# Kernel tuning notes

Hardware: AMD Instinct MI355X
Metric: run time of the kernel (lower is better)

The kernel has to match this reference:

```python
import jax, jax.numpy as jnp
import numpy as np

NUM_TAGS = 16
PAD, START, STOP = 0, 14, 15
EMBED, HIDDEN = 300, 300
HALF = HIDDEN // 2  # per-direction hidden size
B, T, VOCAB = 64, 512, 50000
NEG = -10000.0


def _lstm_dir(x, mask, Wih, Whh, bih, bhh, reverse):
    # x: (B,T,D) float, mask: (B,T) float 0/1. Mask-gated state emulates packed sequences.
    h0 = jnp.zeros((x.shape[0], Whh.shape[1]), x.dtype)

    def step(carry, inp):
        h, c = carry
        xt, mt = inp
        gates = xt @ Wih.T + bih + h @ Whh.T + bhh  # (B, 4*HALF)
        i, f, g, o = jnp.split(gates, 4, axis=-1)  # torch gate order i,f,g,o
        c_new = jax.nn.sigmoid(f) * c + jax.nn.sigmoid(i) * jnp.tanh(g)
        h_new = jax.nn.sigmoid(o) * jnp.tanh(c_new)
        m = mt[:, None]
        h = m * h_new + (1.0 - m) * h
        c = m * c_new + (1.0 - m) * c
        return (h, c), h

    xs = (jnp.swapaxes(x, 0, 1), jnp.swapaxes(mask, 0, 1))
    _, hs = jax.lax.scan(step, (h0, h0), xs, reverse=reverse)
    return jnp.swapaxes(hs, 0, 1)  # (B,T,HALF)


def _bilstm(x, mask, Wih, Whh, bih, bhh):
    fwd = _lstm_dir(x, mask, Wih[0], Whh[0], bih[0], bhh[0], False)
    bwd = _lstm_dir(x, mask, Wih[1], Whh[1], bih[1], bhh[1], True)
    return jnp.concatenate([fwd, bwd], axis=-1)  # (B,T,HIDDEN)


def _crf_partition(h, mask, trans):
    # Forward algorithm: log-sum-exp recurrence over tags.
    alpha = jnp.full((h.shape[0], NUM_TAGS), NEG, h.dtype).at[:, START].set(0.0)

    def step(alpha, inp):
        ht, mt = inp  # ht: (B,K), mt: (B,)
        # scores[b, next, prev] = alpha[b,prev] + emission[b,next] + trans[next,prev]
        a_new = jax.nn.logsumexp(alpha[:, None, :] + ht[:, :, None] + trans[None], axis=-1)
        m = mt[:, None]
        return a_new * m + alpha * (1.0 - m), None

    alpha, _ = jax.lax.scan(step, alpha, (jnp.swapaxes(h, 0, 1), jnp.swapaxes(mask, 0, 1)))
    return jax.nn.logsumexp(alpha + trans[STOP], axis=-1)  # (B,)


def _crf_score(h, y, mask, trans):
    # Gold path score, fully vectorized (original loops per batch element).
    b = h.shape[0]
    y_ext = jnp.concatenate([jnp.full((b, 1), START, dtype=y.dtype), y], axis=1)  # (B,T+1)
    em = jnp.take_along_axis(h, y_ext[:, 1:, None], axis=2)[..., 0]  # (B,T)
    tr = trans[y_ext[:, 1:], y_ext[:, :-1]]  # (B,T)
    score = jnp.sum((em + tr) * mask, axis=1)
    lengths = jnp.sum(mask, axis=1).astype(jnp.int32)
    last = jnp.take_along_axis(y_ext, lengths[:, None], axis=1)[:, 0]
    return score + trans[STOP, last]


def _forward(x, y, embed_weight, Wih0, Whh0, bih0, bhh0, Wih1, Whh1, bih1, bhh1, Wout, bout, transition):
    mask = (x > 0).astype(jnp.float32)
    e = embed_weight[x]  # (B,T,EMBED); PAD row is zeros
    h1 = _bilstm(e, mask, Wih0, Whh0, bih0, bhh0)
    h2 = _bilstm(h1, mask, Wih1, Whh1, bih1, bhh1)
    emis = (h2 @ Wout.T + bout) * mask[..., None]  # (B,T,NUM_TAGS)
    Z = _crf_partition(emis, mask, transition)
    s = _crf_score(emis, y, mask, transition)
    return Z - s  # per-example NLL, shape (B,)


def setup_inputs():
    key = jax.random.key(0)
    ks = jax.random.split(key, 16)
    lengths = jax.random.randint(ks[0], (B,), T // 4, T + 1)
    mask = jnp.arange(T)[None, :] < lengths[:, None]
    x = jnp.where(mask, jax.random.randint(ks[1], (B, T), 1, VOCAB), 0).astype(jnp.int32)
    y = jnp.where(mask, jax.random.randint(ks[2], (B, T), 1, 14), 0).astype(jnp.int32)
    embed_weight = jax.random.normal(ks[3], (VOCAB, EMBED), jnp.float32).at[PAD].set(0.0)
    s = 1.0 / float(np.sqrt(HALF))

    def u(k, shape):
        return jax.random.uniform(k, shape, jnp.float32, -s, s)

    Wih0 = u(ks[4], (2, 4 * HALF, EMBED))
    Whh0 = u(ks[5], (2, 4 * HALF, HALF))
    bih0 = u(ks[6], (2, 4 * HALF))
    bhh0 = u(ks[7], (2, 4 * HALF))
    Wih1 = u(ks[8], (2, 4 * HALF, HIDDEN))
    Whh1 = u(ks[9], (2, 4 * HALF, HALF))
    bih1 = u(ks[10], (2, 4 * HALF))
    bhh1 = u(ks[11], (2, 4 * HALF))
    Wout = u(ks[12], (NUM_TAGS, HIDDEN))
    bout = u(ks[13], (NUM_TAGS,))
    tr = jax.random.normal(ks[14], (NUM_TAGS, NUM_TAGS), jnp.float32)
    tr = tr.at[START, :].set(NEG).at[:, STOP].set(NEG).at[:, PAD].set(NEG).at[PAD, :].set(NEG)
    tr = tr.at[PAD, STOP].set(0.0).at[PAD, PAD].set(0.0)
    return {"x": x, "y": y, "embed_weight": embed_weight,
            "Wih0": Wih0, "Whh0": Whh0, "bih0": bih0, "bhh0": bhh0,
            "Wih1": Wih1, "Whh1": Whh1, "bih1": bih1, "bhh1": bhh1,
            "Wout": Wout, "bout": bout, "transition": tr}


def reference(x, y, embed_weight, Wih0, Whh0, bih0, bhh0, Wih1, Whh1, bih1, bhh1, Wout, bout, transition):
    return _forward(x, y, embed_weight, Wih0, Whh0, bih0, bhh0, Wih1, Whh1, bih1, bhh1, Wout, bout, transition)
```

## Files before the change

### kernel.cpp

```cpp
#include <hip/hip_runtime.h>
#include <hip/hip_bf16.h>

#define TB 512
#define NB 64
#define HID 300
#define HHALF 150
#define G4 600
#define KP 320
#define MTOT (NB*TB)
#define NTAG 16
#define NEGV -10000.0f

using short8 = __attribute__((ext_vector_type(8))) short;
using f32x4  = __attribute__((ext_vector_type(4))) float;
using u32x8  = __attribute__((ext_vector_type(8))) unsigned;
using u32x4  = __attribute__((ext_vector_type(4))) unsigned;
using half2v = __attribute__((ext_vector_type(2))) _Float16;

__device__ __forceinline__ unsigned short f2bf(float f){
  union { float f; unsigned u; } v; v.f = f;
  unsigned r = v.u + 0x7FFFu + ((v.u >> 16) & 1u);
  return (unsigned short)(r >> 16);
}
__device__ __forceinline__ float fsig(float x){ return __fdividef(1.f, 1.f + __expf(-x)); }
__device__ __forceinline__ float ftanh(float x){ return 1.f - __fdividef(2.f, __expf(2.f*x) + 1.f); }

__device__ __forceinline__ unsigned pkh(float a, float b){
  _Float16 ha = (_Float16)a, hb = (_Float16)b;
  unsigned short ua, ub;
  __builtin_memcpy(&ua, &ha, 2); __builtin_memcpy(&ub, &hb, 2);
  return (unsigned)ua | ((unsigned)ub << 16);
}
__device__ __forceinline__ float dot2(unsigned w, unsigned h, float acc){
  half2v wv, hv;
  __builtin_memcpy(&wv, &w, 4); __builtin_memcpy(&hv, &h, 4);
  return __builtin_amdgcn_fdot2(wv, hv, acc, false);
}

__device__ __forceinline__ void bar_lds(){
  asm volatile("s_waitcnt lgkmcnt(0)" ::: "memory");
  __builtin_amdgcn_s_barrier();
  asm volatile("" ::: "memory");
}

__global__ void k_gather_embed(const int* __restrict__ x, const float* __restrict__ emb,
                               unsigned short* __restrict__ Abf){
  long long total = (long long)MTOT * KP;
  for (long long idx = (long long)blockIdx.x*blockDim.x + threadIdx.x; idx < total;
       idx += (long long)gridDim.x*blockDim.x){
    int m = (int)(idx / KP), k = (int)(idx % KP);
    float v = 0.f;
    if (k < HID) v = emb[(long long)x[m]*HID + k];
    Abf[idx] = f2bf(v);
  }
}

__global__ void k_cvt_h(const float* __restrict__ h, unsigned short* __restrict__ Abf){
  long long total = (long long)MTOT * KP;
  for (long long idx = (long long)blockIdx.x*blockDim.x + threadIdx.x; idx < total;
       idx += (long long)gridDim.x*blockDim.x){
    int m = (int)(idx / KP), k = (int)(idx % KP);
    Abf[idx] = f2bf(k < HID ? h[(long long)m*HID + k] : 0.f);
  }
}

__global__ void k_cvt_w(const float* __restrict__ Wih, const float* __restrict__ bih,
                        const float* __restrict__ bhh,
                        unsigned short* __restrict__ Wbf, float* __restrict__ bsum){
  int idx = blockIdx.x*blockDim.x + threadIdx.x;
  if (idx >= 1216*KP) return;
  int n = idx / KP, k = idx % KP;
  float v = (n < 1200 && k < HID) ? Wih[(long long)n*HID + k] : 0.f;
  Wbf[idx] = f2bf(v);
  if (k == 0) bsum[n] = (n < 1200) ? (bih[n] + bhh[n]) : 0.f;
}

__global__ __launch_bounds__(256) void k_proj(const unsigned short* __restrict__ A,
                                              const unsigned short* __restrict__ Wb,
                                              const float* __restrict__ bsum,
                                              float* __restrict__ pre){
  int m0 = blockIdx.x * 128;
  int n0 = blockIdx.y * 64;
  int wid = threadIdx.x >> 6, lane = threadIdx.x & 63;
  int la = lane & 15, lk = lane >> 4;
  int mw = m0 + wid*32;
  f32x4 acc[2][4];
  #pragma unroll
  for (int i=0;i<2;i++){
    #pragma unroll
    for (int j=0;j<4;j++){ acc[i][j][0]=0.f; acc[i][j][1]=0.f; acc[i][j][2]=0.f; acc[i][j][3]=0.f; }
  }
  const unsigned short* Ap = A  + (long long)(mw + la)*KP + lk*8;
  const unsigned short* Bp = Wb + (long long)(n0 + la)*KP + lk*8;
  #pragma unroll 2
  for (int kk=0; kk<KP; kk+=32){
    short8 a0 = *(const short8*)(Ap + kk);
    short8 a1 = *(const short8*)(Ap + 16*KP + kk);
    short8 b0 = *(const short8*)(Bp + kk);
    short8 b1 = *(const short8*)(Bp + 16*KP + kk);
    short8 b2 = *(const short8*)(Bp + 32*KP + kk);
    short8 b3 = *(const short8*)(Bp + 48*KP + kk);
    acc[0][0] = __builtin_amdgcn_mfma_f32_16x16x32_bf16(a0,b0,acc[0][0],0,0,0);
    acc[0][1] = __builtin_amdgcn_mfma_f32_16x16x32_bf16(a0,b1,acc[0][1],0,0,0);
    acc[0][2] = __builtin_amdgcn_mfma_f32_16x16x32_bf16(a0,b2,acc[0][2],0,0,0);
    acc[0][3] = __builtin_amdgcn_mfma_f32_16x16x32_bf16(a0,b3,acc[0][3],0,0,0);
    acc[1][0] = __builtin_amdgcn_mfma_f32_16x16x32_bf16(a1,b0,acc[1][0],0,0,0);
    acc[1][1] = __builtin_amdgcn_mfma_f32_16x16x32_bf16(a1,b1,acc[1][1],0,0,0);
    acc[1][2] = __builtin_amdgcn_mfma_f32_16x16x32_bf16(a1,b2,acc[1][2],0,0,0);
    acc[1][3] = __builtin_amdgcn_mfma_f32_16x16x32_bf16(a1,b3,acc[1][3],0,0,0);
  }
  #pragma unroll
  for (int ms=0; ms<2; ms++){
    #pragma unroll
    for (int ns=0; ns<4; ns++){
      int n = n0 + ns*16 + la;
      if (n < 1200){
        int dir = (n >= 600) ? 1 : 0;
        int j = n - dir*600;
        float bs = bsum[n];
        #pragma unroll
        for (int r=0;r<4;r++){
          int row = mw + ms*16 + lk*4 + r;
          pre[((long long)dir*MTOT + row)*G4 + j] = acc[ms][ns][r] + bs;
        }
      }
    }
  }
}

#define MK8(P,B) (u32x8){ pkh(P[(B)],P[(B)+1]), pkh(P[(B)+2],P[(B)+3]), \
  pkh(P[(B)+4],P[(B)+5]), pkh(P[(B)+6],P[(B)+7]), pkh(P[(B)+8],P[(B)+9]), \
  pkh(P[(B)+10],P[(B)+11]), pkh(P[(B)+12],P[(B)+13]), pkh(P[(B)+14],P[(B)+15]) }
#define MK4T(P) (u32x4){ pkh(P[144],P[145]), pkh(P[146],P[147]), pkh(P[148],P[149]), 0u }
#define DOTQ(hq, W0, E0, W1, E1) { u32x4 hv = hp[(hq)]; \
  a0 = dot2(W0[(E0)+0], hv.x, a0); b0 = dot2(W0[(E0)+1], hv.y, b0); \
  a0 = dot2(W0[(E0)+2], hv.z, a0); b0 = dot2(W0[(E0)+3], hv.w, b0); \
  a1 = dot2(W1[(E1)+0], hv.x, a1); b1 = dot2(W1[(E1)+1], hv.y, b1); \
  a1 = dot2(W1[(E1)+2], hv.z, a1); b1 = dot2(W1[(E1)+3], hv.w, b1); }

__global__ __launch_bounds__(320, 1) void k_rec(const float* __restrict__ pre,
                                                const float* __restrict__ Whh,
                                                const int* __restrict__ x,
                                                float* __restrict__ hout){
  int dir = blockIdx.x >> 6;
  int b   = blockIdx.x & 63;
  int tid = threadIdx.x;
  __shared__ __align__(16) unsigned short h16[152];
  __shared__ float g_lds[G4];
  __shared__ int   x_lds[TB];
  const float* wr0 = Whh + (long long)(dir*G4 + tid)*HHALF;
  const float* wr1 = wr0 + 300*HHALF;
  u32x8 w0_0,w0_1,w0_2,w0_3,w0_4,w0_5,w0_6,w0_7,w0_8;
  u32x8 w1_0,w1_1,w1_2,w1_3,w1_4,w1_5,w1_6,w1_7,w1_8;
  u32x4 w0_9, w1_9;
  if (tid < 300){
    w0_0=MK8(wr0,0);   w0_1=MK8(wr0,16);  w0_2=MK8(wr0,32);  w0_3=MK8(wr0,48);
    w0_4=MK8(wr0,64);  w0_5=MK8(wr0,80);  w0_6=MK8(wr0,96);  w0_7=MK8(wr0,112);
    w0_8=MK8(wr0,128); w0_9=MK4T(wr0);
    w1_0=MK8(wr1,0);   w1_1=MK8(wr1,16);  w1_2=MK8(wr1,32);  w1_3=MK8(wr1,48);
    w1_4=MK8(wr1,64);  w1_5=MK8(wr1,80);  w1_6=MK8(wr1,96);  w1_7=MK8(wr1,112);
    w1_8=MK8(wr1,128); w1_9=MK4T(wr1);
  } else {
    w0_0=(u32x8)(0u);w0_1=(u32x8)(0u);w0_2=(u32x8)(0u);w0_3=(u32x8)(0u);
    w0_4=(u32x8)(0u);w0_5=(u32x8)(0u);w0_6=(u32x8)(0u);w0_7=(u32x8)(0u);
    w0_8=(u32x8)(0u);w0_9=(u32x4)(0u);
    w1_0=(u32x8)(0u);w1_1=(u32x8)(0u);w1_2=(u32x8)(0u);w1_3=(u32x8)(0u);
    w1_4=(u32x8)(0u);w1_5=(u32x8)(0u);w1_6=(u32x8)(0u);w1_7=(u32x8)(0u);
    w1_8=(u32x8)(0u);w1_9=(u32x4)(0u);
  }
  if (tid < 152) h16[tid] = 0;
  for (int q = tid; q < TB; q += 320) x_lds[q] = x[b*TB + q];
  float c = 0.f, hreg = 0.f;
  int jj = (tid < 300) ? tid : 0;
  const float* preB = pre + ((long long)dir*MTOT + (long long)b*TB)*G4;
  float* hb = hout + (long long)b*TB*HID + dir*HHALF + tid;
  const u32x4* hp = (const u32x4*)h16;
  int t0 = dir ? (TB-1) : 0;
  float pv0_c = preB[(long long)t0*G4 + jj];
  float pv1_c = preB[(long long)t0*G4 + jj + 300];
  bar_lds();
  #pragma unroll 1
  for (int s=0; s<TB; s++){
    int t = dir ? (TB-1-s) : s;
    int sn = (s+1 < TB) ? (s+1) : s;
    int tn = dir ? (TB-1-sn) : sn;
    float pv0_n = preB[(long long)tn*G4 + jj];
    float pv1_n = preB[(long long)tn*G4 + jj + 300];
    int xv = x_lds[t];
    if (xv > 0){
      if (tid < 300){
        float a0=0.f, b0=0.f, a1=0.f, b1=0.f;
        DOTQ(0,  w0_0,0, w1_0,0) DOTQ(1,  w0_0,4, w1_0,4)
        DOTQ(2,  w0_1,0, w1_1,0) DOTQ(3,  w0_1,4, w1_1,4)
        DOTQ(4,  w0_2,0, w1_2,0) DOTQ(5,  w0_2,4, w1_2,4)
        DOTQ(6,  w0_3,0, w1_3,0) DOTQ(7,  w0_3,4, w1_3,4)
        DOTQ(8,  w0_4,0, w1_4,0) DOTQ(9,  w0_4,4, w1_4,4)
        DOTQ(10, w0_5,0, w1_5,0) DOTQ(11, w0_5,4, w1_5,4)
        DOTQ(12, w0_6,0, w1_6,0) DOTQ(13, w0_6,4, w1_6,4)
        DOTQ(14, w0_7,0, w1_7,0) DOTQ(15, w0_7,4, w1_7,4)
        DOTQ(16, w0_8,0, w1_8,0) DOTQ(17, w0_8,4, w1_8,4)
        DOTQ(18, w0_9,0, w1_9,0)
        g_lds[tid]       = pv0_c + (a0 + b0);
        g_lds[tid + 300] = pv1_c + (a1 + b1);
      }
      bar_lds();
      if (tid < HHALF){
        float ig = g_lds[tid], fg = g_lds[HHALF+tid], gg = g_lds[2*HHALF+tid], og = g_lds[3*HHALF+tid];
        float cn = fsig(fg)*c + fsig(ig)*ftanh(gg);
        float hn = fsig(og)*ftanh(cn);
        _Float16 hh = (_Float16)hn;
        unsigned short hu; __builtin_memcpy(&hu, &hh, 2);
        h16[tid] = hu;
        c = cn; hreg = hn;
        hb[(long long)t*HID] = hn;
      }
      bar_lds();
    } else {
      if (tid < HHALF) hb[(long long)t*HID] = hreg;
    }
    pv0_c = pv0_n; pv1_c = pv1_n;
  }
}

__global__ __launch_bounds__(256) void k_emis(const float* __restrict__ h2,
                                              const float* __restrict__ Wout,
                                              const float* __restrict__ bout,
                                              const int* __restrict__ x,
                                              float* __restrict__ emis){
  int m = blockIdx.x*16 + (threadIdx.x >> 4);
  int n = threadIdx.x & 15;
  const float* hr = h2 + (long long)m*HID;
  const float* wr = Wout + n*HID;
  float acc = 0.f;
  #pragma unroll 4
  for (int k=0;k<HID;k++) acc += hr[k]*wr[k];
  float mm = (x[m] > 0) ? 1.f : 0.f;
  emis[(long long)m*NTAG + n] = (acc + bout[n]) * mm;
}

__global__ __launch_bounds__(64) void k_crf_part(const float* __restrict__ emis,
                                                 const float* __restrict__ trans,
                                                 const int* __restrict__ x,
                                                 float* __restrict__ out){
  int b = blockIdx.x;
  int lane = threadIdx.x;
  int i = lane & 15, q = lane >> 4;
  float t0 = trans[i*16 + q*4 + 0];
  float t1 = trans[i*16 + q*4 + 1];
  float t2 = trans[i*16 + q*4 + 2];
  float t3 = trans[i*16 + q*4 + 3];
  float al = (i == 14) ? 0.f : NEGV;
  const float* eb = emis + (long long)b*TB*NTAG + i;
  const int* xb = x + b*TB;
  float ht_n = eb[0];
  int   xv_n = xb[0];
  #pragma unroll 1
  for (int t=0; t<TB; t++){
    float ht = ht_n; int xv = xv_n;
    if (t+1 < TB){ ht_n = eb[(t+1)*NTAG]; xv_n = xb[t+1]; }
    if (xv > 0){
      float a0 = __shfl(al, q*4+0);
      float a1 = __shfl(al, q*4+1);
      float a2 = __shfl(al, q*4+2);
      float a3 = __shfl(al, q*4+3);
      float v0 = a0+t0, v1 = a1+t1, v2 = a2+t2, v3 = a3+t3;
      float mx = fmaxf(fmaxf(v0,v1), fmaxf(v2,v3));
      mx = fmaxf(mx, __shfl_xor(mx, 16));
      mx = fmaxf(mx, __shfl_xor(mx, 32));
      float sm = __expf(v0-mx) + __expf(v1-mx) + __expf(v2-mx) + __expf(v3-mx);
      sm += __shfl_xor(sm, 16);
      sm += __shfl_xor(sm, 32);
      al = mx + __logf(sm) + ht;
    }
  }
  float av = (lane < 16) ? (al + trans[15*16 + lane]) : -3.0e38f;
  float mx = av;
  mx = fmaxf(mx, __shfl_xor(mx, 1));
  mx = fmaxf(mx, __shfl_xor(mx, 2));
  mx = fmaxf(mx, __shfl_xor(mx, 4));
  mx = fmaxf(mx, __shfl_xor(mx, 8));
  float sm = (lane < 16) ? __expf(av - mx) : 0.f;
  sm += __shfl_xor(sm, 1);
  sm += __shfl_xor(sm, 2);
  sm += __shfl_xor(sm, 4);
  sm += __shfl_xor(sm, 8);
  if (lane == 0) out[b] = mx + __logf(sm);
}

__global__ __launch_bounds__(64) void k_crf_score(const float* __restrict__ emis,
                                                  const float* __restrict__ trans,
                                                  const int* __restrict__ x,
                                                  const int* __restrict__ y,
                                                  float* __restrict__ out){
  int b = blockIdx.x;
  int lane = threadIdx.x;
  float part = 0.f; int cnt = 0;
  for (int t = lane; t < TB; t += 64){
    if (x[b*TB + t] > 0){
      int yt = y[b*TB + t];
      int prev = (t == 0) ? 14 : y[b*TB + t - 1];
      part += emis[((long long)b*TB + t)*NTAG + yt] + trans[yt*16 + prev];
      cnt++;
    }
  }
  #pragma unroll
  for (int d=1; d<64; d<<=1){ part += __shfl_xor(part, d); cnt += __shfl_xor(cnt, d); }
  if (lane == 0){
    int last = (cnt == 0) ? 14 : y[b*TB + cnt - 1];
    out[b] -= (part + trans[15*16 + last]);
  }
}

extern "C" void kernel_launch(void* const* d_in, const int* in_sizes, int n_in,
                              void* d_out, int out_size, void* d_ws, size_t ws_size,
                              hipStream_t stream){
  const int*   x     = (const int*)d_in[0];
  const int*   y     = (const int*)d_in[1];
  const float* emb   = (const float*)d_in[2];
  const float* Wih0  = (const float*)d_in[3];
  const float* Whh0  = (const float*)d_in[4];
  const float* bih0  = (const float*)d_in[5];
  const float* bhh0  = (const float*)d_in[6];
  const float* Wih1  = (const float*)d_in[7];
  const float* Whh1  = (const float*)d_in[8];
  const float* bih1  = (const float*)d_in[9];
  const float* bhh1  = (const float*)d_in[10];
  const float* Wout  = (const float*)d_in[11];
  const float* bout  = (const float*)d_in[12];
  const float* trans = (const float*)d_in[13];
  float* out = (float*)d_out;

  char* ws = (char*)d_ws;
  size_t off = 0;
  auto alloc = [&](size_t n){ char* p = ws + off; off = (off + n + 255) & ~(size_t)255; return p; };
  unsigned short* Abf  = (unsigned short*)alloc((size_t)MTOT*KP*2);
  unsigned short* Wbf0 = (unsigned short*)alloc((size_t)1216*KP*2);
  unsigned short* Wbf1 = (unsigned short*)alloc((size_t)1216*KP*2);
  float* bsum0 = (float*)alloc(1216*4);
  float* bsum1 = (float*)alloc(1216*4);
  float* pre   = (float*)alloc((size_t)2*MTOT*G4*4);
  float* h1    = (float*)alloc((size_t)MTOT*HID*4);
  float* h2    = (float*)alloc((size_t)MTOT*HID*4);
  float* emis  = (float*)alloc((size_t)MTOT*NTAG*4);

  hipLaunchKernelGGL(k_cvt_w, dim3(1520), dim3(256), 0, stream, Wih0, bih0, bhh0, Wbf0, bsum0);
  hipLaunchKernelGGL(k_cvt_w, dim3(1520), dim3(256), 0, stream, Wih1, bih1, bhh1, Wbf1, bsum1);
  hipLaunchKernelGGL(k_gather_embed, dim3(4096), dim3(256), 0, stream, x, emb, Abf);
  hipLaunchKernelGGL(k_proj, dim3(256,19), dim3(256), 0, stream, Abf, Wbf0, bsum0, pre);
  hipLaunchKernelGGL(k_rec, dim3(128), dim3(320), 0, stream, pre, Whh0, x, h1);
  hipLaunchKernelGGL(k_cvt_h, dim3(4096), dim3(256), 0, stream, h1, Abf);
  hipLaunchKernelGGL(k_proj, dim3(256,19), dim3(256), 0, stream, Abf, Wbf1, bsum1, pre);
  hipLaunchKernelGGL(k_rec, dim3(128), dim3(320), 0, stream, pre, Whh1, x, h2);
  hipLaunchKernelGGL(k_emis, dim3(2048), dim3(256), 0, stream, h2, Wout, bout, x, emis);
  hipLaunchKernelGGL(k_crf_part, dim3(64), dim3(64), 0, stream, emis, trans, x, out);
  hipLaunchKernelGGL(k_crf_score, dim3(64), dim3(64), 0, stream, emis, trans, x, y, out);
}
```

Measured before the change: 1.773 ms.

## Remap LSTM gate rows to thread pairs and double-buffer hidden state

After: 1.910 ms. 7.7% more time.

```diff
diff --git a/kernel.cpp b/kernel.cpp
--- a/kernel.cpp
+++ b/kernel.cpp
@@ -145,15 +145,19 @@
   int dir = blockIdx.x >> 6;
   int b   = blockIdx.x & 63;
   int tid = threadIdx.x;
-  __shared__ __align__(16) unsigned short h16[152];
-  __shared__ float g_lds[G4];
-  __shared__ int   x_lds[TB];
-  const float* wr0 = Whh + (long long)(dir*G4 + tid)*HHALF;
-  const float* wr1 = wr0 + 300*HHALF;
+  int act = (tid < 300);
+  int m   = act ? (tid >> 1) : 0;
+  int sub = tid & 1;
+  __shared__ __align__(16) unsigned short h16[2][152];
+  __shared__ int x_lds[TB];
+  int rA = m + sub*300;
+  int rB = m + 150 + sub*300;
+  const float* wr0 = Whh + (long long)(dir*G4 + rA)*HHALF;
+  const float* wr1 = Whh + (long long)(dir*G4 + rB)*HHALF;
   u32x8 w0_0,w0_1,w0_2,w0_3,w0_4,w0_5,w0_6,w0_7,w0_8;
   u32x8 w1_0,w1_1,w1_2,w1_3,w1_4,w1_5,w1_6,w1_7,w1_8;
   u32x4 w0_9, w1_9;
-  if (tid < 300){
+  if (act){
     w0_0=MK8(wr0,0);   w0_1=MK8(wr0,16);  w0_2=MK8(wr0,32);  w0_3=MK8(wr0,48);
     w0_4=MK8(wr0,64);  w0_5=MK8(wr0,80);  w0_6=MK8(wr0,96);  w0_7=MK8(wr0,112);
     w0_8=MK8(wr0,128); w0_9=MK4T(wr0);
@@ -168,56 +172,55 @@
     w1_4=(u32x8)(0u);w1_5=(u32x8)(0u);w1_6=(u32x8)(0u);w1_7=(u32x8)(0u);
     w1_8=(u32x8)(0u);w1_9=(u32x4)(0u);
   }
-  if (tid < 152) h16[tid] = 0;
+  if (tid < 152){ h16[0][tid] = 0; h16[1][tid] = 0; }
   for (int q = tid; q < TB; q += 320) x_lds[q] = x[b*TB + q];
   float c = 0.f, hreg = 0.f;
-  int jj = (tid < 300) ? tid : 0;
   const float* preB = pre + ((long long)dir*MTOT + (long long)b*TB)*G4;
-  float* hb = hout + (long long)b*TB*HID + dir*HHALF + tid;
-  const u32x4* hp = (const u32x4*)h16;
+  float* hb = hout + (long long)b*TB*HID + dir*HHALF + m;
   int t0 = dir ? (TB-1) : 0;
-  float pv0_c = preB[(long long)t0*G4 + jj];
-  float pv1_c = preB[(long long)t0*G4 + jj + 300];
+  float pv0_c = preB[(long long)t0*G4 + rA];
+  float pv1_c = preB[(long long)t0*G4 + rB];
   bar_lds();
   #pragma unroll 1
   for (int s=0; s<TB; s++){
     int t = dir ? (TB-1-s) : s;
     int sn = (s+1 < TB) ? (s+1) : s;
     int tn = dir ? (TB-1-sn) : sn;
-    float pv0_n = preB[(long long)tn*G4 + jj];
-    float pv1_n = preB[(long long)tn*G4 + jj + 300];
+    float pv0_n = preB[(long long)tn*G4 + rA];
+    float pv1_n = preB[(long long)tn*G4 + rB];
     int xv = x_lds[t];
     if (xv > 0){
-      if (tid < 300){
-        float a0=0.f, b0=0.f, a1=0.f, b1=0.f;
-        DOTQ(0,  w0_0,0, w1_0,0) DOTQ(1,  w0_0,4, w1_0,4)
-        DOTQ(2,  w0_1,0, w1_1,0) DOTQ(3,  w0_1,4, w1_1,4)
-        DOTQ(4,  w0_2,0, w1_2,0) DOTQ(5,  w0_2,4, w1_2,4)
-        DOTQ(6,  w0_3,0, w1_3,0) DOTQ(7,  w0_3,4, w1_3,4)
-        DOTQ(8,  w0_4,0, w1_4,0) DOTQ(9,  w0_4,4, w1_4,4)
-        DOTQ(10, w0_5,0, w1_5,0) DOTQ(11, w0_5,4, w1_5,4)
-        DOTQ(12, w0_6,0, w1_6,0) DOTQ(13, w0_6,4, w1_6,4)
-        DOTQ(14, w0_7,0, w1_7,0) DOTQ(15, w0_7,4, w1_7,4)
-        DOTQ(16, w0_8,0, w1_8,0) DOTQ(17, w0_8,4, w1_8,4)
-        DOTQ(18, w0_9,0, w1_9,0)
-        g_lds[tid]       = pv0_c + (a0 + b0);
-        g_lds[tid + 300] = pv1_c + (a1 + b1);
-      }
-      bar_lds();
-      if (tid < HHALF){
-        float ig = g_lds[tid], fg = g_lds[HHALF+tid], gg = g_lds[2*HHALF+tid], og = g_lds[3*HHALF+tid];
-        float cn = fsig(fg)*c + fsig(ig)*ftanh(gg);
-        float hn = fsig(og)*ftanh(cn);
-        _Float16 hh = (_Float16)hn;
-        unsigned short hu; __builtin_memcpy(&hu, &hh, 2);
-        h16[tid] = hu;
-        c = cn; hreg = hn;
-        hb[(long long)t*HID] = hn;
-      }
-      bar_lds();
-    } else {
-      if (tid < HHALF) hb[(long long)t*HID] = hreg;
-    }
+      const u32x4* hp = (const u32x4*)h16[s & 1];
+      float a0=0.f, b0=0.f, a1=0.f, b1=0.f;
+      DOTQ(0,  w0_0,0, w1_0,0) DOTQ(1,  w0_0,4, w1_0,4)
+      DOTQ(2,  w0_1,0, w1_1,0) DOTQ(3,  w0_1,4, w1_1,4)
+      DOTQ(4,  w0_2,0, w1_2,0) DOTQ(5,  w0_2,4, w1_2,4)
+      DOTQ(6,  w0_3,0, w1_3,0) DOTQ(7,  w0_3,4, w1_3,4)
+      DOTQ(8,  w0_4,0, w1_4,0) DOTQ(9,  w0_4,4, w1_4,4)
+      DOTQ(10, w0_5,0, w1_5,0) DOTQ(11, w0_5,4, w1_5,4)
+      DOTQ(12, w0_6,0, w1_6,0) DOTQ(13, w0_6,4, w1_6,4)
+      DOTQ(14, w0_7,0, w1_7,0) DOTQ(15, w0_7,4, w1_7,4)
+      DOTQ(16, w0_8,0, w1_8,0) DOTQ(17, w0_8,4, w1_8,4)
+      DOTQ(18, w0_9,0, w1_9,0)
+      float gA = pv0_c + (a0 + b0);
+      float gB = pv1_c + (a1 + b1);
+      float pA = __shfl_xor(gA, 1);
+      float pB = __shfl_xor(gB, 1);
+      float ig = sub ? pA : gA;
+      float fg = sub ? pB : gB;
+      float gg = sub ? gA : pA;
+      float og = sub ? gB : pB;
+      float cn = fsig(fg)*c + fsig(ig)*ftanh(gg);
+      float hn = fsig(og)*ftanh(cn);
+      c = cn; hreg = hn;
+    }
+    if (act & (sub == 0)){
+      _Float16 hh = (_Float16)hreg;
+      unsigned short hu; __builtin_memcpy(&hu, &hh, 2);
+      h16[(s+1) & 1][m] = hu;
+      hb[(long long)t*HID] = hreg;
+    }
+    bar_lds();
     pv0_c = pv0_n; pv1_c = pv1_n;
   }
 }
```
